# Kernel tuning notes

Hardware: AMD Instinct MI355X
Metric: run time of the kernel (lower is better)

## Reference

```python
import jax, jax.numpy as jnp
import numpy as np
from math import log2

N_QUBITS = 11
N_LAYERS = 2
DEGREE = 3
N_TIMESTEPS = 8
BSZ = 64
DIM = 2 ** N_QUBITS
N_ROTS = 4 * N_QUBITS * N_LAYERS  # 88


def _ry(theta):
    # batched RY(theta): (B,) -> (B,2,2) complex64
    h = 0.5 * theta
    c, s = jnp.cos(h), jnp.sin(h)
    U = jnp.stack([jnp.stack([c, -s], -1), jnp.stack([s, c], -1)], -2)
    return U.astype(jnp.complex64)


def _rx(theta):
    # batched RX(theta): (B,) -> (B,2,2) complex64
    h = 0.5 * theta
    c = jnp.cos(h).astype(jnp.complex64)
    s = (-1j) * jnp.sin(h).astype(jnp.complex64)
    return jnp.stack([jnp.stack([c, s], -1), jnp.stack([s, c], -1)], -2)


def _apply_1q(state, U, w):
    # state: (B,) + (2,)*n ; apply per-batch 2x2 U on wire w
    s = jnp.moveaxis(state, w + 1, 1)
    shp = s.shape
    s = s.reshape(shp[0], 2, -1)
    s = jnp.einsum('bij,bjr->bir', U, s)
    return jnp.moveaxis(s.reshape(shp), 1, w + 1)


def _apply_crx(state, theta, c_w, t_w):
    # controlled-RX: apply RX on target wire t_w where control wire c_w is |1>
    U = _rx(theta)
    s = jnp.moveaxis(state, (c_w + 1, t_w + 1), (1, 2))
    shp = s.shape
    s = s.reshape(shp[0], 2, 2, -1)
    s1 = jnp.einsum('bij,bjr->bir', U, s[:, 1])
    s = jnp.concatenate([s[:, :1], s1[:, None]], axis=1).reshape(shp)
    return jnp.moveaxis(s, (1, 2), (c_w + 1, t_w + 1))


def _sim14_evolve(state, params):
    # faithful sim14_circuit (v3 fixed RY-CRX gate set), batched angles
    n = state.ndim - 1
    layers = params.shape[1] // (4 * n)
    idx = 0
    for _ in range(layers):
        for i in range(n):
            state = _apply_1q(state, _ry(params[:, idx]), i); idx += 1
        for i in range(n - 1, -1, -1):
            state = _apply_crx(state, params[:, idx], i, (i + 1) % n); idx += 1
        for i in range(n):
            state = _apply_1q(state, _ry(params[:, idx]), i); idx += 1
        for i in [n - 1] + list(range(n - 1)):
            state = _apply_crx(state, params[:, idx], i, (i - 1) % n); idx += 1
    return state


def _apply_unitaries(base, uparams, coeffs):
    # apply_unitaries_pl: repeat_interleave + evolve + LCU einsum
    bsz, T, n_rots = uparams.shape
    dim = base.shape[1]
    n = int(round(log2(dim)))
    flat = uparams.reshape(bsz * T, n_rots)
    rep = jnp.repeat(base, T, axis=0).reshape((bsz * T,) + (2,) * n)
    ev = _sim14_evolve(rep, flat).reshape(bsz, T, dim)
    return jnp.einsum('bti,bt->bi', ev, coeffs.astype(jnp.complex64))


def setup_inputs() -> dict:
    key = jax.random.key(0)
    k1, k2, k3, k4 = jax.random.split(key, 4)
    base_states = jax.random.normal(k1, (BSZ, DIM), dtype=jnp.float32)
    unitary_params = jax.random.normal(k2, (BSZ, N_TIMESTEPS, N_ROTS), dtype=jnp.float32)
    lcu_coeffs = jax.random.normal(k3, (BSZ, N_TIMESTEPS), dtype=jnp.float32)
    poly_coeffs = jax.random.normal(k4, (DEGREE + 1,), dtype=jnp.float32)
    return {"base_states": base_states, "unitary_params": unitary_params,
            "lcu_coeffs": lcu_coeffs, "poly_coeffs": poly_coeffs}


def reference(base_states, unitary_params, lcu_coeffs, poly_coeffs):
    # evaluate_polynomial_state_pl (QSVT polynomial state preparation)
    base = base_states.astype(jnp.complex64)
    base = base / jnp.linalg.norm(base, axis=1, keepdims=True)  # valid quantum state
    pc = poly_coeffs.astype(jnp.complex64)
    acc = pc[0] * base
    working = base
    for k in range(1, poly_coeffs.shape[0]):
        working = _apply_unitaries(working, unitary_params, lcu_coeffs)
        acc = acc + pc[k] * working
    out = acc / jnp.sum(jnp.abs(poly_coeffs)).astype(jnp.complex64)
    # return real/imag stacked so output is real-valued: (bsz, dim, 2)
    return jnp.stack([out.real, out.imag], axis=-1)
```

## Files before the change

kernel.cpp:

```cpp
#include <hip/hip_runtime.h>
#include <utility>

#define DIM 2048
#define NQ 11
#define NROT 88
#define BSZ 64
#define NT 8
#define NPC 4

constexpr int g_type(int G) {
    int j = G % 44;
    return (j < 11 || (j >= 22 && j < 33)) ? 0 : 1;
}
constexpr int g_pt(int G) {
    int j = G % 44;
    if (j < 11) return 10 - j;
    if (j < 22) { int i = 21 - j; int tw = (i + 1 == NQ) ? 0 : i + 1; return 10 - tw; }
    if (j < 33) return 10 - (j - 22);
    if (j == 33) return 1;
    int i = j - 34; int tw = (i + 10) % NQ; return 10 - tw;
}
constexpr int g_pcb(int G) {
    int j = G % 44;
    if (j >= 11 && j < 22) { int i = 21 - j; return 10 - i; }
    if (j == 33) return 0;
    if (j >= 34) { int i = j - 34; return 10 - i; }
    return 0;
}

template<int LB>
__device__ __forceinline__ float lane_xor(float x) {
    if constexpr (LB == 0) {
        return __int_as_float(__builtin_amdgcn_update_dpp(
            __float_as_int(x), __float_as_int(x), 0xB1, 0xF, 0xF, true));
    } else if constexpr (LB == 1) {
        return __int_as_float(__builtin_amdgcn_update_dpp(
            __float_as_int(x), __float_as_int(x), 0x4E, 0xF, 0xF, true));
    } else if constexpr (LB == 2) {
        return __int_as_float(__builtin_amdgcn_ds_swizzle(__float_as_int(x), 0x101F));
    } else if constexpr (LB == 3) {
        return __int_as_float(__builtin_amdgcn_ds_swizzle(__float_as_int(x), 0x201F));
    } else if constexpr (LB == 4) {
        return __int_as_float(__builtin_amdgcn_ds_swizzle(__float_as_int(x), 0x401F));
    } else {
        return __shfl_xor(x, 32, 64);
    }
}

template<int G>
__device__ __forceinline__ void apply_gate(
    float (&sr)[8], float (&si)[8],
    const float* __restrict__ sc, const float* __restrict__ ss,
    float* __restrict__ exr, float* __restrict__ exi, const int tid)
{
    constexpr int type = g_type(G);
    constexpr int pt   = g_pt(G);
    constexpr int pcb  = g_pcb(G);
    const float c = sc[G];
    const float s = ss[G];

    if constexpr (pt <= 2) {
        if constexpr (type == 0) {
#pragma unroll
            for (int m = 0; m < 4; ++m) {
                int jl = ((m >> pt) << (pt + 1)) | (m & ((1 << pt) - 1));
                int jh = jl | (1 << pt);
                float lr = sr[jl], hr = sr[jh];
                float li = si[jl], hi = si[jh];
                sr[jl] = c*lr - s*hr;  sr[jh] = s*lr + c*hr;
                si[jl] = c*li - s*hi;  si[jh] = s*li + c*hi;
            }
        } else if constexpr (pcb <= 2) {
#pragma unroll
            for (int m = 0; m < 4; ++m) {
                int jl = ((m >> pt) << (pt + 1)) | (m & ((1 << pt) - 1));
                int jh = jl | (1 << pt);
                if ((jl >> pcb) & 1) {
                    float lr = sr[jl], li = si[jl];
                    float hr = sr[jh], hi = si[jh];
                    sr[jl] = c*lr + s*hi;   si[jl] = c*li - s*hr;
                    sr[jh] = c*hr + s*li;   si[jh] = c*hi - s*lr;
                }
            }
        } else {
            const bool ctrl = (tid >> (pcb - 3)) & 1;
            if (ctrl) {
#pragma unroll
                for (int m = 0; m < 4; ++m) {
                    int jl = ((m >> pt) << (pt + 1)) | (m & ((1 << pt) - 1));
                    int jh = jl | (1 << pt);
                    float lr = sr[jl], li = si[jl];
                    float hr = sr[jh], hi = si[jh];
                    sr[jl] = c*lr + s*hi;   si[jl] = c*li - s*hr;
                    sr[jh] = c*hr + s*li;   si[jh] = c*hi - s*lr;
                }
            }
        }
    } else if constexpr (pt <= 8) {
        constexpr int lb = pt - 3;
        if constexpr (type == 0) {
            const float sg = ((tid >> lb) & 1) ? s : -s;
#pragma unroll
            for (int j = 0; j < 8; ++j) {
                float pr = lane_xor<lb>(sr[j]);
                float pi = lane_xor<lb>(si[j]);
                sr[j] = c*sr[j] + sg*pr;
                si[j] = c*si[j] + sg*pi;
            }
        } else if constexpr (pcb <= 2) {
#pragma unroll
            for (int j = 0; j < 8; ++j) {
                if ((j >> pcb) & 1) {
                    float pr = lane_xor<lb>(sr[j]);
                    float pi = lane_xor<lb>(si[j]);
                    float nr = c*sr[j] + s*pi;
                    float ni = c*si[j] - s*pr;
                    sr[j] = nr; si[j] = ni;
                }
            }
        } else {
            const bool ctrl = (tid >> (pcb - 3)) & 1;
            if (ctrl) {
#pragma unroll
                for (int j = 0; j < 8; ++j) {
                    float pr = lane_xor<lb>(sr[j]);
                    float pi = lane_xor<lb>(si[j]);
                    float nr = c*sr[j] + s*pi;
                    float ni = c*si[j] - s*pr;
                    sr[j] = nr; si[j] = ni;
                }
            }
        }
    } else {
        const int ptid = tid ^ (1 << (pt - 3));
#pragma unroll
        for (int j = 0; j < 8; ++j) { exr[j*256+tid] = sr[j]; exi[j*256+tid] = si[j]; }
        __syncthreads();
        if constexpr (type == 0) {
            const float sg = ((tid >> (pt - 3)) & 1) ? s : -s;
#pragma unroll
            for (int j = 0; j < 8; ++j) {
                float pr = exr[j*256+ptid], pi = exi[j*256+ptid];
                sr[j] = c*sr[j] + sg*pr;
                si[j] = c*si[j] + sg*pi;
            }
        } else if constexpr (pcb <= 2) {
#pragma unroll
            for (int j = 0; j < 8; ++j) {
                if ((j >> pcb) & 1) {
                    float pr = exr[j*256+ptid], pi = exi[j*256+ptid];
                    float nr = c*sr[j] + s*pi;
                    float ni = c*si[j] - s*pr;
                    sr[j] = nr; si[j] = ni;
                }
            }
        } else {
            const bool ctrl = (tid >> (pcb - 3)) & 1;
            if (ctrl) {
#pragma unroll
                for (int j = 0; j < 8; ++j) {
                    float pr = exr[j*256+ptid], pi = exi[j*256+ptid];
                    float nr = c*sr[j] + s*pi;
                    float ni = c*si[j] - s*pr;
                    sr[j] = nr; si[j] = ni;
                }
            }
        }
        __syncthreads();
    }
}

template<int... Gs>
__device__ __forceinline__ void apply_all(std::integer_sequence<int, Gs...>,
    float (&sr)[8], float (&si)[8],
    const float* __restrict__ sc, const float* __restrict__ ss,
    float* __restrict__ exr, float* __restrict__ exi, const int tid)
{
    (apply_gate<Gs>(sr, si, sc, ss, exr, exi, tid), ...);
}

__global__ __launch_bounds__(256) void setup_kernel(
    const float* __restrict__ base, const float* __restrict__ pc,
    float2* __restrict__ working, float2* __restrict__ acc)
{
    int b = blockIdx.x;
    int tid = threadIdx.x;
    __shared__ float red[4];
    float ssum = 0.f;
    for (int i = tid; i < DIM; i += 256) {
        float v = base[b * DIM + i];
        ssum += v * v;
    }
    for (int off = 32; off > 0; off >>= 1) ssum += __shfl_down(ssum, off, 64);
    if ((tid & 63) == 0) red[tid >> 6] = ssum;
    __syncthreads();
    if (tid == 0) red[0] = red[0] + red[1] + red[2] + red[3];
    __syncthreads();
    float inv = rsqrtf(red[0]);
    float p0 = pc[0];
    for (int i = tid; i < DIM; i += 256) {
        float v = base[b * DIM + i] * inv;
        working[b * DIM + i] = make_float2(v, 0.f);
        acc[b * DIM + i] = make_float2(p0 * v, 0.f);
    }
}

__global__ __launch_bounds__(256) void evolve_kernel(
    const float2* __restrict__ working, const float* __restrict__ uparams,
    const float* __restrict__ lcu, float2* __restrict__ partial, int tpb)
{
    __shared__ float exr[DIM], exi[DIM];
    __shared__ float sc[NROT], ss[NROT];

    const int nchunks = NT / tpb;
    const int b = blockIdx.x / nchunks;
    const int chunk = blockIdx.x - b * nchunks;
    const int tid = threadIdx.x;

    float sr[8], si[8], ar[8], ai[8];
#pragma unroll
    for (int j = 0; j < 8; ++j) { ar[j] = 0.f; ai[j] = 0.f; }

    for (int tt = 0; tt < tpb; ++tt) {
        const int t = chunk * tpb + tt;
        __syncthreads();
        if (tid < NROT) {
            float th = 0.5f * uparams[(b * NT + t) * NROT + tid];
            sc[tid] = cosf(th); ss[tid] = sinf(th);
        }
        const float4* wsrc = (const float4*)(working + (size_t)b * DIM);
#pragma unroll
        for (int jj = 0; jj < 4; ++jj) {
            float4 v = wsrc[tid * 4 + jj];
            sr[2*jj]   = v.x; si[2*jj]   = v.y;
            sr[2*jj+1] = v.z; si[2*jj+1] = v.w;
        }
        __syncthreads();

        apply_all(std::make_integer_sequence<int, NROT>{}, sr, si, sc, ss, exr, exi, tid);

        const float coeff = lcu[b * NT + t];
#pragma unroll
        for (int j = 0; j < 8; ++j) { ar[j] += coeff * sr[j]; ai[j] += coeff * si[j]; }
    }

    float4* pdst = (float4*)(partial + ((size_t)b * nchunks + chunk) * DIM);
#pragma unroll
    for (int jj = 0; jj < 4; ++jj) {
        float4 v;
        v.x = ar[2*jj];   v.y = ai[2*jj];
        v.z = ar[2*jj+1]; v.w = ai[2*jj+1];
        pdst[tid * 4 + jj] = v;
    }
}

__global__ __launch_bounds__(256) void reduce_kernel(
    const float2* __restrict__ partial, const float* __restrict__ pcoef,
    float2* __restrict__ working, float2* __restrict__ acc,
    float* __restrict__ out, int nchunks, int k, int last)
{
    int b = blockIdx.x >> 3;
    int i = ((blockIdx.x & 7) << 8) | threadIdx.x;
    float pk = pcoef[k];
    float sr = 0.f, si = 0.f;
    for (int c = 0; c < nchunks; ++c) {
        float2 v = partial[((size_t)b * nchunks + c) * DIM + i];
        sr += v.x; si += v.y;
    }
    working[b * DIM + i] = make_float2(sr, si);
    float2 a = acc[b * DIM + i];
    a.x += pk * sr; a.y += pk * si;
    acc[b * DIM + i] = a;
    if (last) {
        float sabs = 0.f;
        for (int q = 0; q < NPC; ++q) sabs += fabsf(pcoef[q]);
        float invn = 1.0f / sabs;
        out[((size_t)b * DIM + i) * 2 + 0] = a.x * invn;
        out[((size_t)b * DIM + i) * 2 + 1] = a.y * invn;
    }
}

extern "C" void kernel_launch(void* const* d_in, const int* in_sizes, int n_in,
                              void* d_out, int out_size, void* d_ws, size_t ws_size,
                              hipStream_t stream) {
    const float* base = (const float*)d_in[0];
    const float* upar = (const float*)d_in[1];
    const float* lcu  = (const float*)d_in[2];
    const float* pc   = (const float*)d_in[3];
    float* out = (float*)d_out;

    const size_t plane = (size_t)BSZ * DIM * sizeof(float2);
    char* ws = (char*)d_ws;
    float2* working = (float2*)ws;
    float2* acc     = (float2*)(ws + plane);
    float2* partial = (float2*)(ws + 2 * plane);

    int tpb = 1;
    while (tpb < NT && 2 * plane + (size_t)(NT / tpb) * plane > ws_size) tpb <<= 1;
    int nchunks = NT / tpb;

    setup_kernel<<<BSZ, 256, 0, stream>>>(base, pc, working, acc);
    for (int k = 1; k <= NPC - 1; ++k) {
        evolve_kernel<<<BSZ * nchunks, 256, 0, stream>>>(working, upar, lcu, partial, tpb);
        reduce_kernel<<<BSZ * 8, 256, 0, stream>>>(partial, pc, working, acc, out,
                                                   nchunks, k, (k == NPC - 1) ? 1 : 0);
    }
}
```

Measured before the change: 102.1 us.

## Fuse partial reduction into evolve kernel and double-buffer LDS exchange

Removes the separate reduce kernels by having each evolve launch sum the previous stage's per-timestep partials itself, with chunk 0 updating the accumulator, and adds a small final kernel. The state is remapped so the lowest qubit bits sit inside float2 pairs. The LDS exchange now packs real and imaginary parts into float4, uses two alternating buffers so one barrier per gate can be dropped, and skips threads whose control bit is off. The cost is redundant partial reads by all eight timestep blocks per batch and more workspace, with a fallback to the old path when the workspace is too small.

```diff
diff --git a/kernel.cpp b/kernel.cpp
--- a/kernel.cpp
+++ b/kernel.cpp
@@ -25,22 +25,27 @@
     if (j >= 11 && j < 22) { int i = 21 - j; return 10 - i; }
     if (j == 33) return 0;
     if (j >= 34) { int i = j - 34; return 10 - i; }
-    return 0;
-}
-
-template<int LB>
-__device__ __forceinline__ float lane_xor(float x) {
-    if constexpr (LB == 0) {
+    return -1;
+}
+constexpr int block_parity(int G) {
+    int c = 0;
+    for (int g = 0; g < G; ++g) if (g_pt(g) >= 9) c ^= 1;
+    return c;
+}
+
+template<int PT>
+__device__ __forceinline__ float lx(float x) {
+    if constexpr (PT == 3) {
         return __int_as_float(__builtin_amdgcn_update_dpp(
             __float_as_int(x), __float_as_int(x), 0xB1, 0xF, 0xF, true));
-    } else if constexpr (LB == 1) {
+    } else if constexpr (PT == 4) {
         return __int_as_float(__builtin_amdgcn_update_dpp(
             __float_as_int(x), __float_as_int(x), 0x4E, 0xF, 0xF, true));
-    } else if constexpr (LB == 2) {
+    } else if constexpr (PT == 5) {
         return __int_as_float(__builtin_amdgcn_ds_swizzle(__float_as_int(x), 0x101F));
-    } else if constexpr (LB == 3) {
+    } else if constexpr (PT == 6) {
         return __int_as_float(__builtin_amdgcn_ds_swizzle(__float_as_int(x), 0x201F));
-    } else if constexpr (LB == 4) {
+    } else if constexpr (PT == 7) {
         return __int_as_float(__builtin_amdgcn_ds_swizzle(__float_as_int(x), 0x401F));
     } else {
         return __shfl_xor(x, 32, 64);
@@ -49,9 +54,9 @@
 
 template<int G>
 __device__ __forceinline__ void apply_gate(
-    float (&sr)[8], float (&si)[8],
+    float2 (&R)[4], float2 (&I)[4],
     const float* __restrict__ sc, const float* __restrict__ ss,
-    float* __restrict__ exr, float* __restrict__ exi, const int tid)
+    float4* __restrict__ exbuf, const int tid)
 {
     constexpr int type = g_type(G);
     constexpr int pt   = g_pt(G);
@@ -59,27 +64,22 @@
     const float c = sc[G];
     const float s = ss[G];
 
-    if constexpr (pt <= 2) {
+    if constexpr (pt == 0) {
         if constexpr (type == 0) {
 #pragma unroll
             for (int m = 0; m < 4; ++m) {
-                int jl = ((m >> pt) << (pt + 1)) | (m & ((1 << pt) - 1));
-                int jh = jl | (1 << pt);
-                float lr = sr[jl], hr = sr[jh];
-                float li = si[jl], hi = si[jh];
-                sr[jl] = c*lr - s*hr;  sr[jh] = s*lr + c*hr;
-                si[jl] = c*li - s*hi;  si[jh] = s*li + c*hi;
-            }
-        } else if constexpr (pcb <= 2) {
-#pragma unroll
-            for (int m = 0; m < 4; ++m) {
-                int jl = ((m >> pt) << (pt + 1)) | (m & ((1 << pt) - 1));
-                int jh = jl | (1 << pt);
-                if ((jl >> pcb) & 1) {
-                    float lr = sr[jl], li = si[jl];
-                    float hr = sr[jh], hi = si[jh];
-                    sr[jl] = c*lr + s*hi;   si[jl] = c*li - s*hr;
-                    sr[jh] = c*hr + s*li;   si[jh] = c*hi - s*lr;
+                float er = R[m].x, orr = R[m].y, ei = I[m].x, oi = I[m].y;
+                R[m].x = c*er - s*orr;  R[m].y = s*er + c*orr;
+                I[m].x = c*ei - s*oi;   I[m].y = s*ei + c*oi;
+            }
+        } else if constexpr (pcb == 1 || pcb == 2) {
+            constexpr int cb = pcb - 1;
+#pragma unroll
+            for (int m = 0; m < 4; ++m) {
+                if ((m >> cb) & 1) {
+                    float er = R[m].x, orr = R[m].y, ei = I[m].x, oi = I[m].y;
+                    R[m].x = c*er + s*oi;   I[m].x = c*ei - s*orr;
+                    R[m].y = c*orr + s*ei;  I[m].y = c*oi - s*er;
                 }
             }
         } else {
@@ -87,96 +87,161 @@
             if (ctrl) {
 #pragma unroll
                 for (int m = 0; m < 4; ++m) {
-                    int jl = ((m >> pt) << (pt + 1)) | (m & ((1 << pt) - 1));
-                    int jh = jl | (1 << pt);
-                    float lr = sr[jl], li = si[jl];
-                    float hr = sr[jh], hi = si[jh];
-                    sr[jl] = c*lr + s*hi;   si[jl] = c*li - s*hr;
-                    sr[jh] = c*hr + s*li;   si[jh] = c*hi - s*lr;
-                }
-            }
-        }
-    } else if constexpr (pt <= 8) {
-        constexpr int lb = pt - 3;
+                    float er = R[m].x, orr = R[m].y, ei = I[m].x, oi = I[m].y;
+                    R[m].x = c*er + s*oi;   I[m].x = c*ei - s*orr;
+                    R[m].y = c*orr + s*ei;  I[m].y = c*oi - s*er;
+                }
+            }
+        }
+    } else if constexpr (pt <= 2) {
+        constexpr int sb = pt - 1;
         if constexpr (type == 0) {
-            const float sg = ((tid >> lb) & 1) ? s : -s;
-#pragma unroll
-            for (int j = 0; j < 8; ++j) {
-                float pr = lane_xor<lb>(sr[j]);
-                float pi = lane_xor<lb>(si[j]);
-                sr[j] = c*sr[j] + sg*pr;
-                si[j] = c*si[j] + sg*pi;
-            }
-        } else if constexpr (pcb <= 2) {
-#pragma unroll
-            for (int j = 0; j < 8; ++j) {
-                if ((j >> pcb) & 1) {
-                    float pr = lane_xor<lb>(sr[j]);
-                    float pi = lane_xor<lb>(si[j]);
-                    float nr = c*sr[j] + s*pi;
-                    float ni = c*si[j] - s*pr;
-                    sr[j] = nr; si[j] = ni;
+#pragma unroll
+            for (int q = 0; q < 2; ++q) {
+                constexpr int dummy = 0; (void)dummy;
+                int ml = ((q >> sb) << (sb + 1)) | (q & ((1 << sb) - 1));
+                int mh = ml | (1 << sb);
+                float2 lr = R[ml], hr = R[mh], li = I[ml], hi = I[mh];
+                R[ml].x = c*lr.x - s*hr.x;  R[ml].y = c*lr.y - s*hr.y;
+                R[mh].x = s*lr.x + c*hr.x;  R[mh].y = s*lr.y + c*hr.y;
+                I[ml].x = c*li.x - s*hi.x;  I[ml].y = c*li.y - s*hi.y;
+                I[mh].x = s*li.x + c*hi.x;  I[mh].y = s*li.y + c*hi.y;
+            }
+        } else if constexpr (pcb == 0) {
+#pragma unroll
+            for (int q = 0; q < 2; ++q) {
+                int ml = ((q >> sb) << (sb + 1)) | (q & ((1 << sb) - 1));
+                int mh = ml | (1 << sb);
+                float lr = R[ml].y, li = I[ml].y, hr = R[mh].y, hi = I[mh].y;
+                R[ml].y = c*lr + s*hi;   I[ml].y = c*li - s*hr;
+                R[mh].y = c*hr + s*li;   I[mh].y = c*hi - s*lr;
+            }
+        } else if constexpr (pcb == 1 || pcb == 2) {
+            constexpr int cb = pcb - 1;
+#pragma unroll
+            for (int q = 0; q < 2; ++q) {
+                int ml = ((q >> sb) << (sb + 1)) | (q & ((1 << sb) - 1));
+                int mh = ml | (1 << sb);
+                if ((ml >> cb) & 1) {
+                    float2 lr = R[ml], li = I[ml], hr = R[mh], hi = I[mh];
+                    R[ml].x = c*lr.x + s*hi.x;  R[ml].y = c*lr.y + s*hi.y;
+                    I[ml].x = c*li.x - s*hr.x;  I[ml].y = c*li.y - s*hr.y;
+                    R[mh].x = c*hr.x + s*li.x;  R[mh].y = c*hr.y + s*li.y;
+                    I[mh].x = c*hi.x - s*lr.x;  I[mh].y = c*hi.y - s*lr.y;
                 }
             }
         } else {
             const bool ctrl = (tid >> (pcb - 3)) & 1;
             if (ctrl) {
 #pragma unroll
-                for (int j = 0; j < 8; ++j) {
-                    float pr = lane_xor<lb>(sr[j]);
-                    float pi = lane_xor<lb>(si[j]);
-                    float nr = c*sr[j] + s*pi;
-                    float ni = c*si[j] - s*pr;
-                    sr[j] = nr; si[j] = ni;
-                }
-            }
-        }
-    } else {
-        const int ptid = tid ^ (1 << (pt - 3));
-#pragma unroll
-        for (int j = 0; j < 8; ++j) { exr[j*256+tid] = sr[j]; exi[j*256+tid] = si[j]; }
-        __syncthreads();
+                for (int q = 0; q < 2; ++q) {
+                    int ml = ((q >> sb) << (sb + 1)) | (q & ((1 << sb) - 1));
+                    int mh = ml | (1 << sb);
+                    float2 lr = R[ml], li = I[ml], hr = R[mh], hi = I[mh];
+                    R[ml].x = c*lr.x + s*hi.x;  R[ml].y = c*lr.y + s*hi.y;
+                    I[ml].x = c*li.x - s*hr.x;  I[ml].y = c*li.y - s*hr.y;
+                    R[mh].x = c*hr.x + s*li.x;  R[mh].y = c*hr.y + s*li.y;
+                    I[mh].x = c*hi.x - s*lr.x;  I[mh].y = c*hi.y - s*lr.y;
+                }
+            }
+        }
+    } else if constexpr (pt <= 8) {
         if constexpr (type == 0) {
             const float sg = ((tid >> (pt - 3)) & 1) ? s : -s;
 #pragma unroll
-            for (int j = 0; j < 8; ++j) {
-                float pr = exr[j*256+ptid], pi = exi[j*256+ptid];
-                sr[j] = c*sr[j] + sg*pr;
-                si[j] = c*si[j] + sg*pi;
-            }
-        } else if constexpr (pcb <= 2) {
-#pragma unroll
-            for (int j = 0; j < 8; ++j) {
-                if ((j >> pcb) & 1) {
-                    float pr = exr[j*256+ptid], pi = exi[j*256+ptid];
-                    float nr = c*sr[j] + s*pi;
-                    float ni = c*si[j] - s*pr;
-                    sr[j] = nr; si[j] = ni;
+            for (int m = 0; m < 4; ++m) {
+                float prx = lx<pt>(R[m].x), pry = lx<pt>(R[m].y);
+                float pix = lx<pt>(I[m].x), piy = lx<pt>(I[m].y);
+                R[m].x = c*R[m].x + sg*prx;  R[m].y = c*R[m].y + sg*pry;
+                I[m].x = c*I[m].x + sg*pix;  I[m].y = c*I[m].y + sg*piy;
+            }
+        } else if constexpr (pcb == 0) {
+#pragma unroll
+            for (int m = 0; m < 4; ++m) {
+                float pry = lx<pt>(R[m].y), piy = lx<pt>(I[m].y);
+                R[m].y = c*R[m].y + s*piy;
+                I[m].y = c*I[m].y - s*pry;
+            }
+        } else if constexpr (pcb == 1 || pcb == 2) {
+            constexpr int cb = pcb - 1;
+#pragma unroll
+            for (int m = 0; m < 4; ++m) {
+                if ((m >> cb) & 1) {
+                    float prx = lx<pt>(R[m].x), pry = lx<pt>(R[m].y);
+                    float pix = lx<pt>(I[m].x), piy = lx<pt>(I[m].y);
+                    R[m].x = c*R[m].x + s*pix;  R[m].y = c*R[m].y + s*piy;
+                    I[m].x = c*I[m].x - s*prx;  I[m].y = c*I[m].y - s*pry;
                 }
             }
         } else {
             const bool ctrl = (tid >> (pcb - 3)) & 1;
             if (ctrl) {
 #pragma unroll
-                for (int j = 0; j < 8; ++j) {
-                    float pr = exr[j*256+ptid], pi = exi[j*256+ptid];
-                    float nr = c*sr[j] + s*pi;
-                    float ni = c*si[j] - s*pr;
-                    sr[j] = nr; si[j] = ni;
-                }
-            }
+                for (int m = 0; m < 4; ++m) {
+                    float prx = lx<pt>(R[m].x), pry = lx<pt>(R[m].y);
+                    float pix = lx<pt>(I[m].x), piy = lx<pt>(I[m].y);
+                    R[m].x = c*R[m].x + s*pix;  R[m].y = c*R[m].y + s*piy;
+                    I[m].x = c*I[m].x - s*prx;  I[m].y = c*I[m].y - s*pry;
+                }
+            }
+        }
+    } else {
+        constexpr int par = block_parity(G);
+        float4* buf = exbuf + par * 1024;
+        const int ptid = tid ^ (1 << (pt - 3));
+        bool participate = true;
+        if constexpr (type == 1 && pcb >= 3) participate = (tid >> (pcb - 3)) & 1;
+        if (participate) {
+#pragma unroll
+            for (int m = 0; m < 4; ++m)
+                buf[m * 256 + tid] = make_float4(R[m].x, R[m].y, I[m].x, I[m].y);
         }
         __syncthreads();
+        if (participate) {
+            if constexpr (type == 0) {
+                const float sg = ((tid >> (pt - 3)) & 1) ? s : -s;
+#pragma unroll
+                for (int m = 0; m < 4; ++m) {
+                    float4 v = buf[m * 256 + ptid];
+                    R[m].x = c*R[m].x + sg*v.x;  R[m].y = c*R[m].y + sg*v.y;
+                    I[m].x = c*I[m].x + sg*v.z;  I[m].y = c*I[m].y + sg*v.w;
+                }
+            } else if constexpr (pcb == 0) {
+#pragma unroll
+                for (int m = 0; m < 4; ++m) {
+                    float4 v = buf[m * 256 + ptid];
+                    R[m].y = c*R[m].y + s*v.w;
+                    I[m].y = c*I[m].y - s*v.y;
+                }
+            } else if constexpr (pcb == 1 || pcb == 2) {
+                constexpr int cb = pcb - 1;
+#pragma unroll
+                for (int m = 0; m < 4; ++m) {
+                    if ((m >> cb) & 1) {
+                        float4 v = buf[m * 256 + ptid];
+                        R[m].x = c*R[m].x + s*v.z;  R[m].y = c*R[m].y + s*v.w;
+                        I[m].x = c*I[m].x - s*v.x;  I[m].y = c*I[m].y - s*v.y;
+                    }
+                }
+            } else {
+#pragma unroll
+                for (int m = 0; m < 4; ++m) {
+                    float4 v = buf[m * 256 + ptid];
+                    R[m].x = c*R[m].x + s*v.z;  R[m].y = c*R[m].y + s*v.w;
+                    I[m].x = c*I[m].x - s*v.x;  I[m].y = c*I[m].y - s*v.y;
+                }
+            }
+        }
     }
 }
 
 template<int... Gs>
 __device__ __forceinline__ void apply_all(std::integer_sequence<int, Gs...>,
-    float (&sr)[8], float (&si)[8],
+    float2 (&R)[4], float2 (&I)[4],
     const float* __restrict__ sc, const float* __restrict__ ss,
-    float* __restrict__ exr, float* __restrict__ exi, const int tid)
-{
-    (apply_gate<Gs>(sr, si, sc, ss, exr, exi, tid), ...);
+    float4* __restrict__ exbuf, const int tid)
+{
+    (apply_gate<Gs>(R, I, sc, ss, exbuf, tid), ...);
 }
 
 __global__ __launch_bounds__(256) void setup_kernel(
@@ -205,11 +270,14 @@
     }
 }
 
+template<bool FROM_PARTIAL>
 __global__ __launch_bounds__(256) void evolve_kernel(
-    const float2* __restrict__ working, const float* __restrict__ uparams,
-    const float* __restrict__ lcu, float2* __restrict__ partial, int tpb)
-{
-    __shared__ float exr[DIM], exi[DIM];
+    const float2* __restrict__ src, const float* __restrict__ uparams,
+    const float* __restrict__ lcu, float2* __restrict__ pout,
+    const float* __restrict__ pcoef, float2* __restrict__ acc,
+    int kprev, int tpb)
+{
+    __shared__ float4 exbuf[2048];
     __shared__ float sc[NROT], ss[NROT];
 
     const int nchunks = NT / tpb;
@@ -217,9 +285,41 @@
     const int chunk = blockIdx.x - b * nchunks;
     const int tid = threadIdx.x;
 
-    float sr[8], si[8], ar[8], ai[8];
-#pragma unroll
-    for (int j = 0; j < 8; ++j) { ar[j] = 0.f; ai[j] = 0.f; }
+    float2 WR[4], WI[4];
+    if constexpr (FROM_PARTIAL) {
+#pragma unroll
+        for (int m = 0; m < 4; ++m) { WR[m] = make_float2(0.f, 0.f); WI[m] = make_float2(0.f, 0.f); }
+        for (int c = 0; c < NT; ++c) {
+            const float4* p4 = (const float4*)(src + ((size_t)b * NT + c) * DIM);
+#pragma unroll
+            for (int m = 0; m < 4; ++m) {
+                float4 v = p4[tid * 4 + m];
+                WR[m].x += v.x; WI[m].x += v.y; WR[m].y += v.z; WI[m].y += v.w;
+            }
+        }
+        if (kprev > 0 && chunk == 0) {
+            float pk = pcoef[kprev];
+            float4* a4 = (float4*)(acc + (size_t)b * DIM);
+#pragma unroll
+            for (int m = 0; m < 4; ++m) {
+                float4 v = a4[tid * 4 + m];
+                v.x += pk * WR[m].x; v.y += pk * WI[m].x;
+                v.z += pk * WR[m].y; v.w += pk * WI[m].y;
+                a4[tid * 4 + m] = v;
+            }
+        }
+    } else {
+        const float4* p4 = (const float4*)(src + (size_t)b * DIM);
+#pragma unroll
+        for (int m = 0; m < 4; ++m) {
+            float4 v = p4[tid * 4 + m];
+            WR[m].x = v.x; WI[m].x = v.y; WR[m].y = v.z; WI[m].y = v.w;
+        }
+    }
+
+    float2 AR[4], AI[4];
+#pragma unroll
+    for (int m = 0; m < 4; ++m) { AR[m] = make_float2(0.f, 0.f); AI[m] = make_float2(0.f, 0.f); }
 
     for (int tt = 0; tt < tpb; ++tt) {
         const int t = chunk * tpb + tt;
@@ -228,30 +328,45 @@
             float th = 0.5f * uparams[(b * NT + t) * NROT + tid];
             sc[tid] = cosf(th); ss[tid] = sinf(th);
         }
-        const float4* wsrc = (const float4*)(working + (size_t)b * DIM);
-#pragma unroll
-        for (int jj = 0; jj < 4; ++jj) {
-            float4 v = wsrc[tid * 4 + jj];
-            sr[2*jj]   = v.x; si[2*jj]   = v.y;
-            sr[2*jj+1] = v.z; si[2*jj+1] = v.w;
-        }
+        float2 R[4], I[4];
+#pragma unroll
+        for (int m = 0; m < 4; ++m) { R[m] = WR[m]; I[m] = WI[m]; }
         __syncthreads();
 
-        apply_all(std::make_integer_sequence<int, NROT>{}, sr, si, sc, ss, exr, exi, tid);
+        apply_all(std::make_integer_sequence<int, NROT>{}, R, I, sc, ss, exbuf, tid);
 
         const float coeff = lcu[b * NT + t];
 #pragma unroll
-        for (int j = 0; j < 8; ++j) { ar[j] += coeff * sr[j]; ai[j] += coeff * si[j]; }
-    }
-
-    float4* pdst = (float4*)(partial + ((size_t)b * nchunks + chunk) * DIM);
-#pragma unroll
-    for (int jj = 0; jj < 4; ++jj) {
-        float4 v;
-        v.x = ar[2*jj];   v.y = ai[2*jj];
-        v.z = ar[2*jj+1]; v.w = ai[2*jj+1];
-        pdst[tid * 4 + jj] = v;
-    }
+        for (int m = 0; m < 4; ++m) {
+            AR[m].x += coeff * R[m].x;  AR[m].y += coeff * R[m].y;
+            AI[m].x += coeff * I[m].x;  AI[m].y += coeff * I[m].y;
+        }
+    }
+
+    float4* o4 = (float4*)(pout + ((size_t)b * nchunks + chunk) * DIM);
+#pragma unroll
+    for (int m = 0; m < 4; ++m)
+        o4[tid * 4 + m] = make_float4(AR[m].x, AI[m].x, AR[m].y, AI[m].y);
+}
+
+__global__ __launch_bounds__(256) void final_kernel(
+    const float2* __restrict__ partial, const float* __restrict__ pcoef,
+    const float2* __restrict__ acc, float* __restrict__ out)
+{
+    int b = blockIdx.x >> 3;
+    int i = ((blockIdx.x & 7) << 8) | threadIdx.x;
+    float sr = 0.f, si = 0.f;
+    for (int c = 0; c < NT; ++c) {
+        float2 v = partial[((size_t)b * NT + c) * DIM + i];
+        sr += v.x; si += v.y;
+    }
+    float sabs = 0.f;
+    for (int q = 0; q < NPC; ++q) sabs += fabsf(pcoef[q]);
+    float invn = 1.0f / sabs;
+    float pk = pcoef[NPC - 1];
+    float2 a = acc[(size_t)b * DIM + i];
+    out[((size_t)b * DIM + i) * 2 + 0] = (a.x + pk * sr) * invn;
+    out[((size_t)b * DIM + i) * 2 + 1] = (a.y + pk * si) * invn;
 }
 
 __global__ __launch_bounds__(256) void reduce_kernel(
@@ -293,16 +408,25 @@
     char* ws = (char*)d_ws;
     float2* working = (float2*)ws;
     float2* acc     = (float2*)(ws + plane);
-    float2* partial = (float2*)(ws + 2 * plane);
-
-    int tpb = 1;
-    while (tpb < NT && 2 * plane + (size_t)(NT / tpb) * plane > ws_size) tpb <<= 1;
-    int nchunks = NT / tpb;
+    float2* pA      = (float2*)(ws + 2 * plane);
+    float2* pB      = (float2*)(ws + 2 * plane + (size_t)NT * plane);
+    float2* pC      = (float2*)(ws + 2 * plane + (size_t)2 * NT * plane);
 
     setup_kernel<<<BSZ, 256, 0, stream>>>(base, pc, working, acc);
-    for (int k = 1; k <= NPC - 1; ++k) {
-        evolve_kernel<<<BSZ * nchunks, 256, 0, stream>>>(working, upar, lcu, partial, tpb);
-        reduce_kernel<<<BSZ * 8, 256, 0, stream>>>(partial, pc, working, acc, out,
-                                                   nchunks, k, (k == NPC - 1) ? 1 : 0);
-    }
-}
+
+    if (ws_size >= (2 + 3 * (size_t)NT) * plane) {
+        evolve_kernel<false><<<BSZ * NT, 256, 0, stream>>>(working, upar, lcu, pA, pc, acc, 0, 1);
+        evolve_kernel<true ><<<BSZ * NT, 256, 0, stream>>>(pA,      upar, lcu, pB, pc, acc, 1, 1);
+        evolve_kernel<true ><<<BSZ * NT, 256, 0, stream>>>(pB,      upar, lcu, pC, pc, acc, 2, 1);
+        final_kernel<<<BSZ * 8, 256, 0, stream>>>(pC, pc, acc, out);
+    } else {
+        int tpb = 1;
+        while (tpb < NT && 2 * plane + (size_t)(NT / tpb) * plane > ws_size) tpb <<= 1;
+        int nchunks = NT / tpb;
+        for (int k = 1; k <= NPC - 1; ++k) {
+            evolve_kernel<false><<<BSZ * nchunks, 256, 0, stream>>>(working, upar, lcu, pA, pc, acc, 0, tpb);
+            reduce_kernel<<<BSZ * 8, 256, 0, stream>>>(pA, pc, working, acc, out,
+                                                       nchunks, k, (k == NPC - 1) ? 1 : 0);
+        }
+    }
+}
```

After: 101.0 us. No clear change (-1.1%).

## Use 512-thread evolve blocks and fuse normalization and reduction into evolve kernels

Applied to the files above, without the earlier changes.

The evolve kernel now uses 512 threads, each holding 4 amplitudes as float2 pairs. Shared-memory exchanges use float4 stores with double-buffered parity, which removes the trailing barrier per cross-wave gate. Base normalization is fused into the first evolve pass, and the partial-sum reduction plus accumulator update is fused into the next pass's load. This cuts the launch count to four when the workspace is large enough, at the cost of much more workspace, redundant re-reading of the partial planes by each of the 8 timestep blocks, and higher register pressure per block.

```diff
diff --git a/kernel.cpp b/kernel.cpp
--- a/kernel.cpp
+++ b/kernel.cpp
@@ -25,11 +25,16 @@
     if (j >= 11 && j < 22) { int i = 21 - j; return 10 - i; }
     if (j == 33) return 0;
     if (j >= 34) { int i = j - 34; return 10 - i; }
-    return 0;
+    return -1;
+}
+constexpr int block_parity(int G) {
+    int c = 0;
+    for (int g = 0; g < G; ++g) if (g_pt(g) >= 8) c ^= 1;
+    return c;
 }
 
 template<int LB>
-__device__ __forceinline__ float lane_xor(float x) {
+__device__ __forceinline__ float lx(float x) {
     if constexpr (LB == 0) {
         return __int_as_float(__builtin_amdgcn_update_dpp(
             __float_as_int(x), __float_as_int(x), 0xB1, 0xF, 0xF, true));
@@ -49,9 +54,9 @@
 
 template<int G>
 __device__ __forceinline__ void apply_gate(
-    float (&sr)[8], float (&si)[8],
+    float2 (&R)[2], float2 (&I)[2],
     const float* __restrict__ sc, const float* __restrict__ ss,
-    float* __restrict__ exr, float* __restrict__ exi, const int tid)
+    float4* __restrict__ exbuf, const int tid)
 {
     constexpr int type = g_type(G);
     constexpr int pt   = g_pt(G);
@@ -59,124 +64,248 @@
     const float c = sc[G];
     const float s = ss[G];
 
-    if constexpr (pt <= 2) {
+    if constexpr (pt == 0) {
         if constexpr (type == 0) {
 #pragma unroll
-            for (int m = 0; m < 4; ++m) {
-                int jl = ((m >> pt) << (pt + 1)) | (m & ((1 << pt) - 1));
-                int jh = jl | (1 << pt);
-                float lr = sr[jl], hr = sr[jh];
-                float li = si[jl], hi = si[jh];
-                sr[jl] = c*lr - s*hr;  sr[jh] = s*lr + c*hr;
-                si[jl] = c*li - s*hi;  si[jh] = s*li + c*hi;
-            }
-        } else if constexpr (pcb <= 2) {
-#pragma unroll
-            for (int m = 0; m < 4; ++m) {
-                int jl = ((m >> pt) << (pt + 1)) | (m & ((1 << pt) - 1));
-                int jh = jl | (1 << pt);
-                if ((jl >> pcb) & 1) {
-                    float lr = sr[jl], li = si[jl];
-                    float hr = sr[jh], hi = si[jh];
-                    sr[jl] = c*lr + s*hi;   si[jl] = c*li - s*hr;
-                    sr[jh] = c*hr + s*li;   si[jh] = c*hi - s*lr;
+            for (int m = 0; m < 2; ++m) {
+                float er = R[m].x, orr = R[m].y, ei = I[m].x, oi = I[m].y;
+                R[m].x = c*er - s*orr;  R[m].y = s*er + c*orr;
+                I[m].x = c*ei - s*oi;   I[m].y = s*ei + c*oi;
+            }
+        } else if constexpr (pcb == 1) {
+            float er = R[1].x, orr = R[1].y, ei = I[1].x, oi = I[1].y;
+            R[1].x = c*er + s*oi;   I[1].x = c*ei - s*orr;
+            R[1].y = c*orr + s*ei;  I[1].y = c*oi - s*er;
+        } else {
+            const bool ctrl = (tid >> (pcb - 2)) & 1;
+            if (ctrl) {
+#pragma unroll
+                for (int m = 0; m < 2; ++m) {
+                    float er = R[m].x, orr = R[m].y, ei = I[m].x, oi = I[m].y;
+                    R[m].x = c*er + s*oi;   I[m].x = c*ei - s*orr;
+                    R[m].y = c*orr + s*ei;  I[m].y = c*oi - s*er;
                 }
             }
+        }
+    } else if constexpr (pt == 1) {
+        if constexpr (type == 0) {
+            float2 l = R[0], h = R[1], li = I[0], hi = I[1];
+            R[0].x = c*l.x - s*h.x;   R[0].y = c*l.y - s*h.y;
+            R[1].x = s*l.x + c*h.x;   R[1].y = s*l.y + c*h.y;
+            I[0].x = c*li.x - s*hi.x; I[0].y = c*li.y - s*hi.y;
+            I[1].x = s*li.x + c*hi.x; I[1].y = s*li.y + c*hi.y;
+        } else if constexpr (pcb == 0) {
+            float lr = R[0].y, li = I[0].y, hr = R[1].y, hi = I[1].y;
+            R[0].y = c*lr + s*hi;   I[0].y = c*li - s*hr;
+            R[1].y = c*hr + s*li;   I[1].y = c*hi - s*lr;
         } else {
-            const bool ctrl = (tid >> (pcb - 3)) & 1;
-            if (ctrl) {
-#pragma unroll
-                for (int m = 0; m < 4; ++m) {
-                    int jl = ((m >> pt) << (pt + 1)) | (m & ((1 << pt) - 1));
-                    int jh = jl | (1 << pt);
-                    float lr = sr[jl], li = si[jl];
-                    float hr = sr[jh], hi = si[jh];
-                    sr[jl] = c*lr + s*hi;   si[jl] = c*li - s*hr;
-                    sr[jh] = c*hr + s*li;   si[jh] = c*hi - s*lr;
-                }
-            }
-        }
-    } else if constexpr (pt <= 8) {
-        constexpr int lb = pt - 3;
+            const bool ctrl = (tid >> (pcb - 2)) & 1;
+            if (ctrl) {
+                float2 l = R[0], h = R[1], li = I[0], hi = I[1];
+                R[0].x = c*l.x + s*hi.x;  R[0].y = c*l.y + s*hi.y;
+                I[0].x = c*li.x - s*h.x;  I[0].y = c*li.y - s*h.y;
+                R[1].x = c*h.x + s*li.x;  R[1].y = c*h.y + s*li.y;
+                I[1].x = c*hi.x - s*l.x;  I[1].y = c*hi.y - s*l.y;
+            }
+        }
+    } else if constexpr (pt <= 7) {
+        constexpr int lb = pt - 2;
         if constexpr (type == 0) {
             const float sg = ((tid >> lb) & 1) ? s : -s;
 #pragma unroll
-            for (int j = 0; j < 8; ++j) {
-                float pr = lane_xor<lb>(sr[j]);
-                float pi = lane_xor<lb>(si[j]);
-                sr[j] = c*sr[j] + sg*pr;
-                si[j] = c*si[j] + sg*pi;
-            }
-        } else if constexpr (pcb <= 2) {
-#pragma unroll
-            for (int j = 0; j < 8; ++j) {
-                if ((j >> pcb) & 1) {
-                    float pr = lane_xor<lb>(sr[j]);
-                    float pi = lane_xor<lb>(si[j]);
-                    float nr = c*sr[j] + s*pi;
-                    float ni = c*si[j] - s*pr;
-                    sr[j] = nr; si[j] = ni;
+            for (int m = 0; m < 2; ++m) {
+                float prx = lx<lb>(R[m].x), pry = lx<lb>(R[m].y);
+                float pix = lx<lb>(I[m].x), piy = lx<lb>(I[m].y);
+                R[m].x = c*R[m].x + sg*prx;  R[m].y = c*R[m].y + sg*pry;
+                I[m].x = c*I[m].x + sg*pix;  I[m].y = c*I[m].y + sg*piy;
+            }
+        } else if constexpr (pcb == 0) {
+#pragma unroll
+            for (int m = 0; m < 2; ++m) {
+                float pry = lx<lb>(R[m].y), piy = lx<lb>(I[m].y);
+                R[m].y = c*R[m].y + s*piy;
+                I[m].y = c*I[m].y - s*pry;
+            }
+        } else if constexpr (pcb == 1) {
+            float prx = lx<lb>(R[1].x), pry = lx<lb>(R[1].y);
+            float pix = lx<lb>(I[1].x), piy = lx<lb>(I[1].y);
+            R[1].x = c*R[1].x + s*pix;  R[1].y = c*R[1].y + s*piy;
+            I[1].x = c*I[1].x - s*prx;  I[1].y = c*I[1].y - s*pry;
+        } else {
+            const bool ctrl = (tid >> (pcb - 2)) & 1;
+            if (ctrl) {
+#pragma unroll
+                for (int m = 0; m < 2; ++m) {
+                    float prx = lx<lb>(R[m].x), pry = lx<lb>(R[m].y);
+                    float pix = lx<lb>(I[m].x), piy = lx<lb>(I[m].y);
+                    R[m].x = c*R[m].x + s*pix;  R[m].y = c*R[m].y + s*piy;
+                    I[m].x = c*I[m].x - s*prx;  I[m].y = c*I[m].y - s*pry;
                 }
             }
+        }
+    } else {
+        constexpr int par = block_parity(G);
+        float4* buf = exbuf + par * 1024;
+        const int ptid = tid ^ (1 << (pt - 2));
+        if constexpr (type == 0) {
+#pragma unroll
+            for (int m = 0; m < 2; ++m)
+                buf[m * 512 + tid] = make_float4(R[m].x, R[m].y, I[m].x, I[m].y);
+            __syncthreads();
+            const float sg = ((tid >> (pt - 2)) & 1) ? s : -s;
+#pragma unroll
+            for (int m = 0; m < 2; ++m) {
+                float4 v = buf[m * 512 + ptid];
+                R[m].x = c*R[m].x + sg*v.x;  R[m].y = c*R[m].y + sg*v.y;
+                I[m].x = c*I[m].x + sg*v.z;  I[m].y = c*I[m].y + sg*v.w;
+            }
+        } else if constexpr (pcb == 0) {
+            float2* f2 = (float2*)buf;
+#pragma unroll
+            for (int m = 0; m < 2; ++m)
+                f2[m * 512 + tid] = make_float2(R[m].y, I[m].y);
+            __syncthreads();
+#pragma unroll
+            for (int m = 0; m < 2; ++m) {
+                float2 v = f2[m * 512 + ptid];
+                R[m].y = c*R[m].y + s*v.y;
+                I[m].y = c*I[m].y - s*v.x;
+            }
+        } else if constexpr (pcb == 1) {
+            buf[tid] = make_float4(R[1].x, R[1].y, I[1].x, I[1].y);
+            __syncthreads();
+            float4 v = buf[ptid];
+            R[1].x = c*R[1].x + s*v.z;  R[1].y = c*R[1].y + s*v.w;
+            I[1].x = c*I[1].x - s*v.x;  I[1].y = c*I[1].y - s*v.y;
         } else {
-            const bool ctrl = (tid >> (pcb - 3)) & 1;
-            if (ctrl) {
-#pragma unroll
-                for (int j = 0; j < 8; ++j) {
-                    float pr = lane_xor<lb>(sr[j]);
-                    float pi = lane_xor<lb>(si[j]);
-                    float nr = c*sr[j] + s*pi;
-                    float ni = c*si[j] - s*pr;
-                    sr[j] = nr; si[j] = ni;
+            const bool ctrl = (tid >> (pcb - 2)) & 1;
+            if (ctrl) {
+#pragma unroll
+                for (int m = 0; m < 2; ++m)
+                    buf[m * 512 + tid] = make_float4(R[m].x, R[m].y, I[m].x, I[m].y);
+            }
+            __syncthreads();
+            if (ctrl) {
+#pragma unroll
+                for (int m = 0; m < 2; ++m) {
+                    float4 v = buf[m * 512 + ptid];
+                    R[m].x = c*R[m].x + s*v.z;  R[m].y = c*R[m].y + s*v.w;
+                    I[m].x = c*I[m].x - s*v.x;  I[m].y = c*I[m].y - s*v.y;
                 }
             }
         }
-    } else {
-        const int ptid = tid ^ (1 << (pt - 3));
-#pragma unroll
-        for (int j = 0; j < 8; ++j) { exr[j*256+tid] = sr[j]; exi[j*256+tid] = si[j]; }
-        __syncthreads();
-        if constexpr (type == 0) {
-            const float sg = ((tid >> (pt - 3)) & 1) ? s : -s;
-#pragma unroll
-            for (int j = 0; j < 8; ++j) {
-                float pr = exr[j*256+ptid], pi = exi[j*256+ptid];
-                sr[j] = c*sr[j] + sg*pr;
-                si[j] = c*si[j] + sg*pi;
-            }
-        } else if constexpr (pcb <= 2) {
-#pragma unroll
-            for (int j = 0; j < 8; ++j) {
-                if ((j >> pcb) & 1) {
-                    float pr = exr[j*256+ptid], pi = exi[j*256+ptid];
-                    float nr = c*sr[j] + s*pi;
-                    float ni = c*si[j] - s*pr;
-                    sr[j] = nr; si[j] = ni;
-                }
-            }
-        } else {
-            const bool ctrl = (tid >> (pcb - 3)) & 1;
-            if (ctrl) {
-#pragma unroll
-                for (int j = 0; j < 8; ++j) {
-                    float pr = exr[j*256+ptid], pi = exi[j*256+ptid];
-                    float nr = c*sr[j] + s*pi;
-                    float ni = c*si[j] - s*pr;
-                    sr[j] = nr; si[j] = ni;
-                }
-            }
-        }
-        __syncthreads();
     }
 }
 
 template<int... Gs>
 __device__ __forceinline__ void apply_all(std::integer_sequence<int, Gs...>,
-    float (&sr)[8], float (&si)[8],
+    float2 (&R)[2], float2 (&I)[2],
     const float* __restrict__ sc, const float* __restrict__ ss,
-    float* __restrict__ exr, float* __restrict__ exi, const int tid)
-{
-    (apply_gate<Gs>(sr, si, sc, ss, exr, exi, tid), ...);
+    float4* __restrict__ exbuf, const int tid)
+{
+    (apply_gate<Gs>(R, I, sc, ss, exbuf, tid), ...);
+}
+
+template<int MODE>
+__global__ __launch_bounds__(512) void evolve_kernel(
+    const void* __restrict__ src, const float* __restrict__ uparams,
+    const float* __restrict__ lcu, float2* __restrict__ pout,
+    const float* __restrict__ pcoef, float2* __restrict__ acc, int kprev)
+{
+    __shared__ float4 exbuf[2048];
+    __shared__ float sc[NROT], ss[NROT];
+    __shared__ float red[9];
+
+    const int b = blockIdx.x >> 3;
+    const int t = blockIdx.x & 7;
+    const int tid = threadIdx.x;
+
+    float2 R[2], I[2];
+    if constexpr (MODE == 0) {
+        const float4* b4 = (const float4*)((const float*)src + (size_t)b * DIM);
+        float4 v = b4[tid];
+        float loc = v.x*v.x + v.y*v.y + v.z*v.z + v.w*v.w;
+        for (int off = 32; off > 0; off >>= 1) loc += __shfl_down(loc, off, 64);
+        if ((tid & 63) == 0) red[tid >> 6] = loc;
+        __syncthreads();
+        if (tid == 0) { float sm = 0.f; for (int w = 0; w < 8; ++w) sm += red[w]; red[8] = sm; }
+        __syncthreads();
+        const float inv = rsqrtf(red[8]);
+        R[0] = make_float2(v.x * inv, v.y * inv);
+        R[1] = make_float2(v.z * inv, v.w * inv);
+        I[0] = make_float2(0.f, 0.f);
+        I[1] = make_float2(0.f, 0.f);
+        if (t == 0) {
+            const float p0 = pcoef[0];
+            float4* a4 = (float4*)(acc + (size_t)b * DIM);
+            a4[tid*2+0] = make_float4(p0*R[0].x, 0.f, p0*R[0].y, 0.f);
+            a4[tid*2+1] = make_float4(p0*R[1].x, 0.f, p0*R[1].y, 0.f);
+        }
+    } else if constexpr (MODE == 1) {
+        R[0] = R[1] = I[0] = I[1] = make_float2(0.f, 0.f);
+        const float2* s2 = (const float2*)src;
+        for (int cc = 0; cc < NT; ++cc) {
+            const float4* p4 = (const float4*)(s2 + ((size_t)b * NT + cc) * DIM);
+#pragma unroll
+            for (int m = 0; m < 2; ++m) {
+                float4 v = p4[tid*2+m];
+                R[m].x += v.x; I[m].x += v.y; R[m].y += v.z; I[m].y += v.w;
+            }
+        }
+        if (t == 0) {
+            const float pk = pcoef[kprev];
+            float4* a4 = (float4*)(acc + (size_t)b * DIM);
+#pragma unroll
+            for (int m = 0; m < 2; ++m) {
+                float4 v = a4[tid*2+m];
+                v.x += pk * R[m].x; v.y += pk * I[m].x;
+                v.z += pk * R[m].y; v.w += pk * I[m].y;
+                a4[tid*2+m] = v;
+            }
+        }
+    } else {
+        const float2* s2 = (const float2*)src;
+        const float4* p4 = (const float4*)(s2 + (size_t)b * DIM);
+#pragma unroll
+        for (int m = 0; m < 2; ++m) {
+            float4 v = p4[tid*2+m];
+            R[m].x = v.x; I[m].x = v.y; R[m].y = v.z; I[m].y = v.w;
+        }
+    }
+
+    if (tid < NROT) {
+        float th = 0.5f * uparams[(b * NT + t) * NROT + tid];
+        sc[tid] = cosf(th); ss[tid] = sinf(th);
+    }
+    __syncthreads();
+
+    apply_all(std::make_integer_sequence<int, NROT>{}, R, I, sc, ss, exbuf, tid);
+
+    const float coeff = lcu[b * NT + t];
+    float4* o4 = (float4*)(pout + ((size_t)b * NT + t) * DIM);
+#pragma unroll
+    for (int m = 0; m < 2; ++m)
+        o4[tid*2+m] = make_float4(coeff*R[m].x, coeff*I[m].x, coeff*R[m].y, coeff*I[m].y);
+}
+
+__global__ __launch_bounds__(256) void final_kernel(
+    const float2* __restrict__ partial, const float* __restrict__ pcoef,
+    const float2* __restrict__ acc, float* __restrict__ out)
+{
+    int b = blockIdx.x >> 3;
+    int i = ((blockIdx.x & 7) << 8) | threadIdx.x;
+    float sr = 0.f, si = 0.f;
+    for (int c = 0; c < NT; ++c) {
+        float2 v = partial[((size_t)b * NT + c) * DIM + i];
+        sr += v.x; si += v.y;
+    }
+    float sabs = 0.f;
+    for (int q = 0; q < NPC; ++q) sabs += fabsf(pcoef[q]);
+    float invn = 1.0f / sabs;
+    float pk = pcoef[NPC - 1];
+    float2 a = acc[(size_t)b * DIM + i];
+    out[((size_t)b * DIM + i) * 2 + 0] = (a.x + pk * sr) * invn;
+    out[((size_t)b * DIM + i) * 2 + 1] = (a.y + pk * si) * invn;
 }
 
 __global__ __launch_bounds__(256) void setup_kernel(
@@ -205,66 +334,17 @@
     }
 }
 
-__global__ __launch_bounds__(256) void evolve_kernel(
-    const float2* __restrict__ working, const float* __restrict__ uparams,
-    const float* __restrict__ lcu, float2* __restrict__ partial, int tpb)
-{
-    __shared__ float exr[DIM], exi[DIM];
-    __shared__ float sc[NROT], ss[NROT];
-
-    const int nchunks = NT / tpb;
-    const int b = blockIdx.x / nchunks;
-    const int chunk = blockIdx.x - b * nchunks;
-    const int tid = threadIdx.x;
-
-    float sr[8], si[8], ar[8], ai[8];
-#pragma unroll
-    for (int j = 0; j < 8; ++j) { ar[j] = 0.f; ai[j] = 0.f; }
-
-    for (int tt = 0; tt < tpb; ++tt) {
-        const int t = chunk * tpb + tt;
-        __syncthreads();
-        if (tid < NROT) {
-            float th = 0.5f * uparams[(b * NT + t) * NROT + tid];
-            sc[tid] = cosf(th); ss[tid] = sinf(th);
-        }
-        const float4* wsrc = (const float4*)(working + (size_t)b * DIM);
-#pragma unroll
-        for (int jj = 0; jj < 4; ++jj) {
-            float4 v = wsrc[tid * 4 + jj];
-            sr[2*jj]   = v.x; si[2*jj]   = v.y;
-            sr[2*jj+1] = v.z; si[2*jj+1] = v.w;
-        }
-        __syncthreads();
-
-        apply_all(std::make_integer_sequence<int, NROT>{}, sr, si, sc, ss, exr, exi, tid);
-
-        const float coeff = lcu[b * NT + t];
-#pragma unroll
-        for (int j = 0; j < 8; ++j) { ar[j] += coeff * sr[j]; ai[j] += coeff * si[j]; }
-    }
-
-    float4* pdst = (float4*)(partial + ((size_t)b * nchunks + chunk) * DIM);
-#pragma unroll
-    for (int jj = 0; jj < 4; ++jj) {
-        float4 v;
-        v.x = ar[2*jj];   v.y = ai[2*jj];
-        v.z = ar[2*jj+1]; v.w = ai[2*jj+1];
-        pdst[tid * 4 + jj] = v;
-    }
-}
-
 __global__ __launch_bounds__(256) void reduce_kernel(
     const float2* __restrict__ partial, const float* __restrict__ pcoef,
     float2* __restrict__ working, float2* __restrict__ acc,
-    float* __restrict__ out, int nchunks, int k, int last)
+    float* __restrict__ out, int k, int last)
 {
     int b = blockIdx.x >> 3;
     int i = ((blockIdx.x & 7) << 8) | threadIdx.x;
     float pk = pcoef[k];
     float sr = 0.f, si = 0.f;
-    for (int c = 0; c < nchunks; ++c) {
-        float2 v = partial[((size_t)b * nchunks + c) * DIM + i];
+    for (int c = 0; c < NT; ++c) {
+        float2 v = partial[((size_t)b * NT + c) * DIM + i];
         sr += v.x; si += v.y;
     }
     working[b * DIM + i] = make_float2(sr, si);
@@ -291,18 +371,25 @@
 
     const size_t plane = (size_t)BSZ * DIM * sizeof(float2);
     char* ws = (char*)d_ws;
-    float2* working = (float2*)ws;
-    float2* acc     = (float2*)(ws + plane);
-    float2* partial = (float2*)(ws + 2 * plane);
-
-    int tpb = 1;
-    while (tpb < NT && 2 * plane + (size_t)(NT / tpb) * plane > ws_size) tpb <<= 1;
-    int nchunks = NT / tpb;
-
-    setup_kernel<<<BSZ, 256, 0, stream>>>(base, pc, working, acc);
-    for (int k = 1; k <= NPC - 1; ++k) {
-        evolve_kernel<<<BSZ * nchunks, 256, 0, stream>>>(working, upar, lcu, partial, tpb);
-        reduce_kernel<<<BSZ * 8, 256, 0, stream>>>(partial, pc, working, acc, out,
-                                                   nchunks, k, (k == NPC - 1) ? 1 : 0);
-    }
-}
+
+    if (ws_size >= (1 + 3 * (size_t)NT) * plane) {
+        float2* acc = (float2*)ws;
+        float2* pA  = (float2*)(ws + plane);
+        float2* pB  = (float2*)(ws + plane + (size_t)NT * plane);
+        float2* pC  = (float2*)(ws + plane + (size_t)2 * NT * plane);
+        evolve_kernel<0><<<BSZ * NT, 512, 0, stream>>>(base, upar, lcu, pA, pc, acc, 0);
+        evolve_kernel<1><<<BSZ * NT, 512, 0, stream>>>(pA,   upar, lcu, pB, pc, acc, 1);
+        evolve_kernel<1><<<BSZ * NT, 512, 0, stream>>>(pB,   upar, lcu, pC, pc, acc, 2);
+        final_kernel<<<BSZ * 8, 256, 0, stream>>>(pC, pc, acc, out);
+    } else {
+        float2* working = (float2*)ws;
+        float2* acc     = (float2*)(ws + plane);
+        float2* pA      = (float2*)(ws + 2 * plane);
+        setup_kernel<<<BSZ, 256, 0, stream>>>(base, pc, working, acc);
+        for (int k = 1; k <= NPC - 1; ++k) {
+            evolve_kernel<2><<<BSZ * NT, 512, 0, stream>>>(working, upar, lcu, pA, pc, acc, 0);
+            reduce_kernel<<<BSZ * 8, 256, 0, stream>>>(pA, pc, working, acc, out,
+                                                       k, (k == NPC - 1) ? 1 : 0);
+        }
+    }
+}
```

New measurement: 87.17 us. 14.7% less time.
